# Optimization experiments

Measured on AMD Instinct MI355X. Metric: run time of the kernel, lower is better.

Reference implementation:

```python
import jax, jax.numpy as jnp
import numpy as np

EPS = 1e-5


def setup_inputs() -> dict:
    key = jax.random.key(0)
    k1, k2, k3, k4 = jax.random.split(key, 4)
    B, C_in, C_out, N_in = 4, 128, 256, 40962
    N_out = (N_in + 6) // 4  # 10242
    x = jax.random.normal(k1, (B, C_in, N_in), dtype=jnp.float32)
    neigh_orders = jax.random.randint(k2, (N_out * 7,), 0, N_in, dtype=jnp.int64)
    W = jax.random.normal(k3, (C_out, C_in), dtype=jnp.float32) * 0.05
    b = jax.random.normal(k4, (C_out,), dtype=jnp.float32) * 0.05
    gamma = jnp.ones((C_out,), dtype=jnp.float32)
    beta = jnp.zeros((C_out,), dtype=jnp.float32)
    return {"x": x, "neigh_orders": neigh_orders, "W": W, "b": b,
            "gamma": gamma, "beta": beta}


def reference(x, neigh_orders, W, b, gamma, beta):
    B, C, N_in = x.shape
    N_out = (N_in + 6) // 4
    idx = neigh_orders[: N_out * 7]
    # irregular gather: (B, C, N_out*7) -> (B, C, N_out, 7), mean over the 7 neighbors
    g = x[:, :, idx].reshape(B, C, N_out, 7).mean(axis=3)  # (B, C, N_out)
    # 1x1 conv == channel GEMM
    y = jnp.einsum('oc,bcn->bon', W, g) + b[None, :, None]  # (B, C_out, N_out)
    # BatchNorm1d with batch statistics (track_running_stats=False), biased var
    mean = y.mean(axis=(0, 2))
    var = y.var(axis=(0, 2))
    y = (y - mean[None, :, None]) * jax.lax.rsqrt(var[None, :, None] + EPS)
    return gamma[None, :, None] * y + beta[None, :, None]
```

## Files before the change

kernel.cpp:

```cpp
#include <hip/hip_runtime.h>
#include <hip/hip_bf16.h>

#define B_ 4
#define C_IN 128
#define C_OUT 256
#define N_IN 40962
#define N_OUT 10242
#define EPS_ 1e-5f
#define CNT_ ((float)(B_ * N_OUT))

typedef __attribute__((ext_vector_type(8))) short bf16x8;
typedef __attribute__((ext_vector_type(4))) float f32x4;

__device__ __forceinline__ float bf2f(unsigned short u) {
    union { unsigned int i; float f; } c;
    c.i = ((unsigned int)u) << 16;
    return c.f;
}
__device__ __forceinline__ unsigned short f2bf(float f) {
    union { float f; unsigned int i; } c;
    c.f = f;
    unsigned int r = c.i + 0x7FFFu + ((c.i >> 16) & 1u);
    return (unsigned short)(r >> 16);
}

#define IBLK 64
#define NB_I ((N_IN + IBLK - 1) / IBLK)
#define WCONV_BLKS ((C_OUT * C_IN) / 256)

__global__ __launch_bounds__(256) void k_transpose(const float* __restrict__ x,
                                                   unsigned short* __restrict__ xT,
                                                   const float* __restrict__ W,
                                                   unsigned short* __restrict__ Wb) {
    if (blockIdx.x >= B_ * NB_I) {
        int i = (blockIdx.x - B_ * NB_I) * 256 + threadIdx.x;
        Wb[i] = f2bf(W[i]);
        return;
    }
    __shared__ float tile[IBLK][C_IN + 1];
    int b  = blockIdx.x / NB_I;
    int ib = blockIdx.x % NB_I;
    int i0 = ib * IBLK;
    int t = threadIdx.x;
    int lane = t & 63;
    int q = t >> 6;

    const float* xb = x + (size_t)b * C_IN * N_IN;
    int i = i0 + lane;
    if (i < N_IN) {
#pragma unroll
        for (int p = 0; p < 32; p++) {
            int k = p * 4 + q;
            tile[lane][k] = xb[(size_t)k * N_IN + i];
        }
    }
    __syncthreads();

    unsigned short* xTb = xT + (size_t)b * N_IN * C_IN;
#pragma unroll
    for (int p = 0; p < 16; p++) {
        int il = p * 4 + q;
        int gi = i0 + il;
        if (gi < N_IN) {
            int k2 = lane * 2;
            float a = tile[il][k2];
            float c = tile[il][k2 + 1];
            unsigned int pk = (unsigned int)f2bf(a) | ((unsigned int)f2bf(c) << 16);
            *reinterpret_cast<unsigned int*>(xTb + (size_t)gi * C_IN + k2) = pk;
        }
    }
}

#define GNB 16
#define NB_G ((N_OUT + GNB - 1) / GNB)

__global__ __launch_bounds__(256) void k_gather(const unsigned short* __restrict__ xT,
                                                const int* __restrict__ idx,
                                                unsigned short* __restrict__ g) {
    int b  = blockIdx.x / NB_G;
    int nb = blockIdx.x % NB_G;
    int t = threadIdx.x;
    int n = nb * GNB + (t >> 4);
    int c = t & 15;
    if (n >= N_OUT) return;

    const unsigned short* xTb = xT + (size_t)b * N_IN * C_IN;
    const int* ip = idx + 7 * n;
    float s[8];
#pragma unroll
    for (int e = 0; e < 8; e++) s[e] = 0.f;
#pragma unroll
    for (int j = 0; j < 7; j++) {
        int id = ip[j];
        bf16x8 v = *reinterpret_cast<const bf16x8*>(xTb + (size_t)id * C_IN + c * 8);
#pragma unroll
        for (int e = 0; e < 8; e++) s[e] += bf2f((unsigned short)v[e]);
    }
    const float inv7 = 1.0f / 7.0f;
    bf16x8 r;
#pragma unroll
    for (int e = 0; e < 8; e++) r[e] = (short)f2bf(s[e] * inv7);
    *reinterpret_cast<bf16x8*>(g + ((size_t)b * N_OUT + n) * C_IN + c * 8) = r;
}

#define NT2 128
#define NB_N2 ((N_OUT + NT2 - 1) / NT2)
#define NBLK_GS (B_ * NB_N2)

__global__ __launch_bounds__(256, 2) void k_stats_gemm(const unsigned short* __restrict__ g,
                                                       const unsigned short* __restrict__ Wb,
                                                       float* __restrict__ psum) {
    int bid = blockIdx.x;
    int b  = bid / NB_N2;
    int nb = bid % NB_N2;
    int t = threadIdx.x;
    int w = t >> 6, l = t & 63, lr = l & 15, lg = l >> 4;
    int wbase = w * 64;

    bf16x8 afrag[4][4];
#pragma unroll
    for (int mt = 0; mt < 4; mt++)
#pragma unroll
        for (int ks = 0; ks < 4; ks++)
            afrag[mt][ks] = *reinterpret_cast<const bf16x8*>(
                Wb + (size_t)(wbase + mt * 16 + lr) * C_IN + ks * 32 + lg * 8);

    const unsigned short* gb = g + (size_t)b * N_OUT * C_IN;
    float ps1[16], ps2[16];
#pragma unroll
    for (int m = 0; m < 16; m++) { ps1[m] = 0.f; ps2[m] = 0.f; }

    for (int h = 0; h < 2; h++) {
        int n0 = nb * NT2 + h * 64;
        f32x4 acc[4][4];
#pragma unroll
        for (int mt = 0; mt < 4; mt++)
#pragma unroll
            for (int nt = 0; nt < 4; nt++) acc[mt][nt] = (f32x4)(0.0f);

#pragma unroll
        for (int nt = 0; nt < 4; nt++) {
            int n = n0 + nt * 16 + lr;
            const unsigned short* gr = gb + (size_t)((n < N_OUT) ? n : 0) * C_IN;
#pragma unroll
            for (int ks = 0; ks < 4; ks++) {
                bf16x8 bfr = *reinterpret_cast<const bf16x8*>(gr + ks * 32 + lg * 8);
#pragma unroll
                for (int mt = 0; mt < 4; mt++)
                    acc[mt][nt] = __builtin_amdgcn_mfma_f32_16x16x32_bf16(afrag[mt][ks], bfr,
                                                                         acc[mt][nt], 0, 0, 0);
            }
        }
#pragma unroll
        for (int mt = 0; mt < 4; mt++) {
#pragma unroll
            for (int j = 0; j < 4; j++) {
#pragma unroll
                for (int nt = 0; nt < 4; nt++) {
                    int n = n0 + nt * 16 + lr;
                    if (n < N_OUT) {
                        float v = acc[mt][nt][j];
                        ps1[mt * 4 + j] += v;
                        ps2[mt * 4 + j] += v * v;
                    }
                }
            }
        }
    }

    __shared__ float red[2][C_OUT];
#pragma unroll
    for (int m = 0; m < 16; m++) {
        float a = ps1[m], cc = ps2[m];
#pragma unroll
        for (int d = 1; d < 16; d <<= 1) {
            a  += __shfl_xor(a, d, 64);
            cc += __shfl_xor(cc, d, 64);
        }
        if (lr == 0) {
            int mt = m >> 2, j = m & 3;
            int o = wbase + mt * 16 + lg * 4 + j;
            red[0][o] = a;
            red[1][o] = cc;
        }
    }
    __syncthreads();
    float* pb = psum + (size_t)bid * 2 * C_OUT;
    pb[t] = red[0][t];
    pb[C_OUT + t] = red[1][t];
}

__global__ __launch_bounds__(256) void k_stats_final(const float* __restrict__ psum,
                                                     const float* __restrict__ bias,
                                                     const float* __restrict__ gamma,
                                                     const float* __restrict__ beta,
                                                     float* __restrict__ ss) {
    int t = threadIdx.x;
    int w = t >> 6, l = t & 63;
    int o = blockIdx.x * 4 + w;
    float s1 = 0.f, s2 = 0.f;
    for (int i = l; i < NBLK_GS; i += 64) {
        const float* pb = psum + (size_t)i * 2 * C_OUT;
        s1 += pb[o];
        s2 += pb[C_OUT + o];
    }
#pragma unroll
    for (int d = 1; d < 64; d <<= 1) {
        s1 += __shfl_xor(s1, d, 64);
        s2 += __shfl_xor(s2, d, 64);
    }
    if (l == 0) {
        float mz = s1 / CNT_;
        float var = s2 / CNT_ - mz * mz;
        float mean = mz + bias[o];
        float a = gamma[o] * rsqrtf(var + EPS_);
        ss[o] = a;
        ss[C_OUT + o] = beta[o] - a * mz;
    }
}

__global__ __launch_bounds__(256, 2) void k_final_gemm(const unsigned short* __restrict__ g,
                                                       const unsigned short* __restrict__ Wb,
                                                       const float* __restrict__ ss,
                                                       float* __restrict__ out) {
    int bid = blockIdx.x;
    int b  = bid / NB_N2;
    int nb = bid % NB_N2;
    int t = threadIdx.x;
    int w = t >> 6, l = t & 63, lr = l & 15, lg = l >> 4;
    int wbase = w * 64;

    bf16x8 afrag[4][4];
#pragma unroll
    for (int mt = 0; mt < 4; mt++)
#pragma unroll
        for (int ks = 0; ks < 4; ks++)
            afrag[mt][ks] = *reinterpret_cast<const bf16x8*>(
                Wb + (size_t)(wbase + mt * 16 + lr) * C_IN + ks * 32 + lg * 8);

    float sa[16], sh[16];
#pragma unroll
    for (int mt = 0; mt < 4; mt++)
#pragma unroll
        for (int j = 0; j < 4; j++) {
            int o = wbase + mt * 16 + lg * 4 + j;
            sa[mt * 4 + j] = ss[o];
            sh[mt * 4 + j] = ss[C_OUT + o];
        }

    const unsigned short* gb = g + (size_t)b * N_OUT * C_IN;
    float* ob = out + (size_t)b * C_OUT * N_OUT;

    for (int h = 0; h < 2; h++) {
        int n0 = nb * NT2 + h * 64;
        f32x4 acc[4][4];
#pragma unroll
        for (int mt = 0; mt < 4; mt++)
#pragma unroll
            for (int nt = 0; nt < 4; nt++) acc[mt][nt] = (f32x4)(0.0f);

#pragma unroll
        for (int nt = 0; nt < 4; nt++) {
            int n = n0 + nt * 16 + lr;
            const unsigned short* gr = gb + (size_t)((n < N_OUT) ? n : 0) * C_IN;
#pragma unroll
            for (int ks = 0; ks < 4; ks++) {
                bf16x8 bfr = *reinterpret_cast<const bf16x8*>(gr + ks * 32 + lg * 8);
#pragma unroll
                for (int mt = 0; mt < 4; mt++)
                    acc[mt][nt] = __builtin_amdgcn_mfma_f32_16x16x32_bf16(afrag[mt][ks], bfr,
                                                                         acc[mt][nt], 0, 0, 0);
            }
        }

#pragma unroll
        for (int mt = 0; mt < 4; mt++) {
#pragma unroll
            for (int j = 0; j < 4; j++) {
                int o = wbase + mt * 16 + lg * 4 + j;
                float a = sa[mt * 4 + j];
                float s = sh[mt * 4 + j];
#pragma unroll
                for (int nt = 0; nt < 4; nt++) {
                    int n = n0 + nt * 16 + lr;
                    if (n < N_OUT) ob[(size_t)o * N_OUT + n] = a * acc[mt][nt][j] + s;
                }
            }
        }
    }
}

extern "C" void kernel_launch(void* const* d_in, const int* in_sizes, int n_in,
                              void* d_out, int out_size, void* d_ws, size_t ws_size,
                              hipStream_t stream) {
    const float* x     = (const float*)d_in[0];
    const int*   idx   = (const int*)d_in[1];
    const float* W     = (const float*)d_in[2];
    const float* bias  = (const float*)d_in[3];
    const float* gamma = (const float*)d_in[4];
    const float* beta  = (const float*)d_in[5];
    float* out = (float*)d_out;

    const size_t xt_bytes = (size_t)B_ * N_IN * C_IN * sizeof(unsigned short);
    const size_t g_bytes  = (size_t)B_ * N_OUT * C_IN * sizeof(unsigned short);
    const size_t wb_bytes = (size_t)C_OUT * C_IN * sizeof(unsigned short);
    unsigned short* xT = (unsigned short*)d_ws;
    unsigned short* gg = (unsigned short*)((char*)d_ws + xt_bytes);
    unsigned short* Wb = (unsigned short*)((char*)d_ws + xt_bytes + g_bytes);
    float* psum = (float*)((char*)d_ws + xt_bytes + g_bytes + wb_bytes);
    float* ss   = psum + (size_t)NBLK_GS * 2 * C_OUT;

    k_transpose<<<B_ * NB_I + WCONV_BLKS, 256, 0, stream>>>(x, xT, W, Wb);
    k_gather<<<B_ * NB_G, 256, 0, stream>>>(xT, idx, gg);
    k_stats_gemm<<<NBLK_GS, 256, 0, stream>>>(gg, Wb, psum);
    k_stats_final<<<64, 256, 0, stream>>>(psum, bias, gamma, beta, ss);
    k_final_gemm<<<B_ * NB_N2, 256, 0, stream>>>(gg, Wb, ss, out);
}
```

Before: 84.45 us.

## Fuse stats GEMM, stats reduction and final GEMM into one persistent kernel

```diff
diff --git a/kernel.cpp b/kernel.cpp
--- a/kernel.cpp
+++ b/kernel.cpp
@@ -31,8 +31,10 @@
 __global__ __launch_bounds__(256) void k_transpose(const float* __restrict__ x,
                                                    unsigned short* __restrict__ xT,
                                                    const float* __restrict__ W,
-                                                   unsigned short* __restrict__ Wb) {
+                                                   unsigned short* __restrict__ Wb,
+                                                   unsigned int* __restrict__ cnt) {
     if (blockIdx.x >= B_ * NB_I) {
+        if (blockIdx.x == B_ * NB_I && threadIdx.x < 2) cnt[threadIdx.x] = 0;
         int i = (blockIdx.x - B_ * NB_I) * 256 + threadIdx.x;
         Wb[i] = f2bf(W[i]);
         return;
@@ -107,9 +109,19 @@
 #define NB_N2 ((N_OUT + NT2 - 1) / NT2)
 #define NBLK_GS (B_ * NB_N2)
 
-__global__ __launch_bounds__(256, 2) void k_stats_gemm(const unsigned short* __restrict__ g,
+__global__ __launch_bounds__(256, 2) void k_fused_gemm(const unsigned short* __restrict__ g,
                                                        const unsigned short* __restrict__ Wb,
-                                                       float* __restrict__ psum) {
+                                                       const float* __restrict__ bias,
+                                                       const float* __restrict__ gamma,
+                                                       const float* __restrict__ beta,
+                                                       float* __restrict__ psum,
+                                                       float* __restrict__ ss,
+                                                       unsigned int* __restrict__ cnt,
+                                                       float* __restrict__ out) {
+    __shared__ float red[2][C_OUT];
+    __shared__ float lds_a[C_OUT];
+    __shared__ float lds_s[C_OUT];
+
     int bid = blockIdx.x;
     int b  = bid / NB_N2;
     int nb = bid % NB_N2;
@@ -126,6 +138,7 @@
                 Wb + (size_t)(wbase + mt * 16 + lr) * C_IN + ks * 32 + lg * 8);
 
     const unsigned short* gb = g + (size_t)b * N_OUT * C_IN;
+
     float ps1[16], ps2[16];
 #pragma unroll
     for (int m = 0; m < 16; m++) { ps1[m] = 0.f; ps2[m] = 0.f; }
@@ -137,7 +150,6 @@
         for (int mt = 0; mt < 4; mt++)
 #pragma unroll
             for (int nt = 0; nt < 4; nt++) acc[mt][nt] = (f32x4)(0.0f);
-
 #pragma unroll
         for (int nt = 0; nt < 4; nt++) {
             int n = n0 + nt * 16 + lr;
@@ -152,9 +164,9 @@
             }
         }
 #pragma unroll
-        for (int mt = 0; mt < 4; mt++) {
-#pragma unroll
-            for (int j = 0; j < 4; j++) {
+        for (int mt = 0; mt < 4; mt++)
+#pragma unroll
+            for (int j = 0; j < 4; j++)
 #pragma unroll
                 for (int nt = 0; nt < 4; nt++) {
                     int n = n0 + nt * 16 + lr;
@@ -164,11 +176,8 @@
                         ps2[mt * 4 + j] += v * v;
                     }
                 }
-            }
-        }
-    }
-
-    __shared__ float red[2][C_OUT];
+    }
+
 #pragma unroll
     for (int m = 0; m < 16; m++) {
         float a = ps1[m], cc = ps2[m];
@@ -185,72 +194,50 @@
         }
     }
     __syncthreads();
-    float* pb = psum + (size_t)bid * 2 * C_OUT;
-    pb[t] = red[0][t];
-    pb[C_OUT + t] = red[1][t];
-}
-
-__global__ __launch_bounds__(256) void k_stats_final(const float* __restrict__ psum,
-                                                     const float* __restrict__ bias,
-                                                     const float* __restrict__ gamma,
-                                                     const float* __restrict__ beta,
-                                                     float* __restrict__ ss) {
-    int t = threadIdx.x;
-    int w = t >> 6, l = t & 63;
-    int o = blockIdx.x * 4 + w;
-    float s1 = 0.f, s2 = 0.f;
-    for (int i = l; i < NBLK_GS; i += 64) {
-        const float* pb = psum + (size_t)i * 2 * C_OUT;
-        s1 += pb[o];
-        s2 += pb[C_OUT + o];
-    }
-#pragma unroll
-    for (int d = 1; d < 64; d <<= 1) {
-        s1 += __shfl_xor(s1, d, 64);
-        s2 += __shfl_xor(s2, d, 64);
-    }
-    if (l == 0) {
-        float mz = s1 / CNT_;
-        float var = s2 / CNT_ - mz * mz;
-        float mean = mz + bias[o];
-        float a = gamma[o] * rsqrtf(var + EPS_);
-        ss[o] = a;
-        ss[C_OUT + o] = beta[o] - a * mz;
-    }
-}
-
-__global__ __launch_bounds__(256, 2) void k_final_gemm(const unsigned short* __restrict__ g,
-                                                       const unsigned short* __restrict__ Wb,
-                                                       const float* __restrict__ ss,
-                                                       float* __restrict__ out) {
-    int bid = blockIdx.x;
-    int b  = bid / NB_N2;
-    int nb = bid % NB_N2;
-    int t = threadIdx.x;
-    int w = t >> 6, l = t & 63, lr = l & 15, lg = l >> 4;
-    int wbase = w * 64;
-
-    bf16x8 afrag[4][4];
-#pragma unroll
-    for (int mt = 0; mt < 4; mt++)
-#pragma unroll
-        for (int ks = 0; ks < 4; ks++)
-            afrag[mt][ks] = *reinterpret_cast<const bf16x8*>(
-                Wb + (size_t)(wbase + mt * 16 + lr) * C_IN + ks * 32 + lg * 8);
-
-    float sa[16], sh[16];
-#pragma unroll
-    for (int mt = 0; mt < 4; mt++)
-#pragma unroll
-        for (int j = 0; j < 4; j++) {
-            int o = wbase + mt * 16 + lg * 4 + j;
-            sa[mt * 4 + j] = ss[o];
-            sh[mt * 4 + j] = ss[C_OUT + o];
-        }
-
-    const unsigned short* gb = g + (size_t)b * N_OUT * C_IN;
+    {
+        float* pb = psum + (size_t)bid * 2 * C_OUT;
+        pb[t] = red[0][t];
+        pb[C_OUT + t] = red[1][t];
+    }
+    __threadfence();
+    __syncthreads();
+    if (t == 0)
+        __hip_atomic_fetch_add(&cnt[0], 1u, __ATOMIC_RELEASE, __HIP_MEMORY_SCOPE_AGENT);
+
+    if (bid < 64) {
+        if (t == 0) {
+            while (__hip_atomic_load(&cnt[0], __ATOMIC_ACQUIRE, __HIP_MEMORY_SCOPE_AGENT)
+                   < (unsigned)NBLK_GS)
+                __builtin_amdgcn_s_sleep(8);
+        }
+        __syncthreads();
+        int o = bid * 4 + w;
+        float s1 = 0.f, s2 = 0.f;
+        for (int i = l; i < NBLK_GS; i += 64) {
+            const float* pb = psum + (size_t)i * 2 * C_OUT;
+            s1 += pb[o];
+            s2 += pb[C_OUT + o];
+        }
+#pragma unroll
+        for (int d = 1; d < 64; d <<= 1) {
+            s1 += __shfl_xor(s1, d, 64);
+            s2 += __shfl_xor(s2, d, 64);
+        }
+        if (l == 0) {
+            float mz = s1 / CNT_;
+            float var = s2 / CNT_ - mz * mz;
+            float a = gamma[o] * rsqrtf(var + EPS_);
+            ss[o] = a;
+            ss[C_OUT + o] = beta[o] - a * mz;
+        }
+        __threadfence();
+        __syncthreads();
+        if (t == 0)
+            __hip_atomic_fetch_add(&cnt[1], 1u, __ATOMIC_RELEASE, __HIP_MEMORY_SCOPE_AGENT);
+    }
+
     float* ob = out + (size_t)b * C_OUT * N_OUT;
-
+    bool have_ss = false;
     for (int h = 0; h < 2; h++) {
         int n0 = nb * NT2 + h * 64;
         f32x4 acc[4][4];
@@ -258,7 +245,6 @@
         for (int mt = 0; mt < 4; mt++)
 #pragma unroll
             for (int nt = 0; nt < 4; nt++) acc[mt][nt] = (f32x4)(0.0f);
-
 #pragma unroll
         for (int nt = 0; nt < 4; nt++) {
             int n = n0 + nt * 16 + lr;
@@ -273,13 +259,26 @@
             }
         }
 
+        if (!have_ss) {
+            if (t == 0) {
+                while (__hip_atomic_load(&cnt[1], __ATOMIC_ACQUIRE, __HIP_MEMORY_SCOPE_AGENT)
+                       < 64u)
+                    __builtin_amdgcn_s_sleep(8);
+            }
+            __syncthreads();
+            lds_a[t] = ss[t];
+            lds_s[t] = ss[C_OUT + t];
+            __syncthreads();
+            have_ss = true;
+        }
+
 #pragma unroll
         for (int mt = 0; mt < 4; mt++) {
 #pragma unroll
             for (int j = 0; j < 4; j++) {
                 int o = wbase + mt * 16 + lg * 4 + j;
-                float a = sa[mt * 4 + j];
-                float s = sh[mt * 4 + j];
+                float a = lds_a[o];
+                float s = lds_s[o];
 #pragma unroll
                 for (int nt = 0; nt < 4; nt++) {
                     int n = n0 + nt * 16 + lr;
@@ -309,10 +308,9 @@
     unsigned short* Wb = (unsigned short*)((char*)d_ws + xt_bytes + g_bytes);
     float* psum = (float*)((char*)d_ws + xt_bytes + g_bytes + wb_bytes);
     float* ss   = psum + (size_t)NBLK_GS * 2 * C_OUT;
-
-    k_transpose<<<B_ * NB_I + WCONV_BLKS, 256, 0, stream>>>(x, xT, W, Wb);
+    unsigned int* cnt = (unsigned int*)(ss + 2 * C_OUT);
+
+    k_transpose<<<B_ * NB_I + WCONV_BLKS, 256, 0, stream>>>(x, xT, W, Wb, cnt);
     k_gather<<<B_ * NB_G, 256, 0, stream>>>(xT, idx, gg);
-    k_stats_gemm<<<NBLK_GS, 256, 0, stream>>>(gg, Wb, psum);
-    k_stats_final<<<64, 256, 0, stream>>>(psum, bias, gamma, beta, ss);
-    k_final_gemm<<<B_ * NB_N2, 256, 0, stream>>>(gg, Wb, ss, out);
-}
+    k_fused_gemm<<<NBLK_GS, 256, 0, stream>>>(gg, Wb, bias, gamma, beta, psum, ss, cnt, out);
+}
```

After: 146.0 us. 1.73x slower.
